# Kernel tuning notes

Hardware: AMD Instinct MI355X
Metric: run time of the kernel (lower is better)

Reference implementation:

```python
import jax, jax.numpy as jnp
import numpy as np

HIDDEN = 512
TEMPERATURE = float(np.sqrt(HIDDEN))  # scaled-dot temperature
BATCH = 64


def _build_weights(attn_weight, N, K):
    """Vectorized version of get_attn_weight: (S,S,H) with S = N*K+1.
    Regions: 0=same_sample, 1=same_class, 2=diff_class, 3=support->query,
    4=query->support, 5=query->query. Replicates the torch overwrite order."""
    S = N * K + 1
    NK = N * K
    i = jnp.arange(S)[:, None]
    j = jnp.arange(S)[None, :]
    idx = jnp.full((S, S), 2, dtype=jnp.int32)                      # w_diff_class
    idx = jnp.where((i // K) == (j // K), 1, idx)                   # w_same_class
    idx = jnp.where((i < NK) & (j == NK), 3, idx)                   # w_stoquery
    idx = jnp.where(i == j, 0, idx)                                 # w_same_sample (diag)
    idx = jnp.where((i == NK) & (j < NK), 4, idx)                   # w_querytos
    idx = jnp.where((i == NK) & (j == NK), 5, idx)                  # w_query
    return attn_weight[idx]  # (S, S, H)


def setup_inputs() -> dict:
    key = jax.random.key(0)
    kq, kk, kv, kw = jax.random.split(key, 4)
    N, K = 10, 10
    S = N * K + 1  # 101
    q = jax.random.normal(kq, (BATCH, S, HIDDEN), dtype=jnp.float32)
    k = jax.random.normal(kk, (BATCH, S, HIDDEN), dtype=jnp.float32)
    v = jax.random.normal(kv, (BATCH, S, HIDDEN), dtype=jnp.float32)
    bound = float(np.sqrt(6 / 2))
    attn_weight = jax.random.uniform(kw, (6, HIDDEN), dtype=jnp.float32,
                                     minval=-bound, maxval=bound)
    return {"q": q, "k": k, "v": v, "attn_weight": attn_weight, "N": N, "K": K}


def reference(q, k, v, attn_weight, N, K):
    # attn[b,i,j] = softmax_j(q.k^T / temperature)
    scores = jnp.einsum("bih,bjh->bij", q, k) / TEMPERATURE
    attn = jax.nn.softmax(scores, axis=2)  # dropout p=0 (eval) -> identity
    weights = _build_weights(attn_weight, N, K)  # (S,S,H)
    # out[b,i,h] = sum_j attn[b,i,j] * weights[i,j,h] * v[b,j,h]
    out = jnp.einsum("bij,ijh,bjh->bih", attn, weights, v)
    return out, attn
```

## Files before the change

### kernel.cpp

```cpp
#include <hip/hip_runtime.h>
#include <math.h>
#include <stdint.h>

#define BATCH 64
#define SEQ   101
#define HID   512
#define NKQ   100
#define KCLS  10
#define INV_TEMP 0.04419417382415922f

typedef short bf16x8 __attribute__((ext_vector_type(8)));
typedef float f32x4  __attribute__((ext_vector_type(4)));
typedef uint32_t u32x4 __attribute__((ext_vector_type(4)));

__device__ inline uint32_t cvt2(float a, float b) {
    uint32_t r;
    asm("v_cvt_pk_bf16_f32 %0, %1, %2" : "=v"(r) : "v"(a), "v"(b));
    return r;
}
__device__ inline void split_bf16(float x, short& hi, short& lo) {
    uint32_t u = __builtin_bit_cast(uint32_t, x);
    hi = (short)(u >> 16);
    float hf = __builtin_bit_cast(float, u & 0xFFFF0000u);
    float l  = x - hf;
    lo = (short)(__builtin_bit_cast(uint32_t, l) >> 16);
}

#define QST 520

#define OFF_QLO 16640
#define POOLSZ  33280

__global__ __launch_bounds__(512, 2)
void fused_attn(const float* __restrict__ q, const float* __restrict__ k,
                const float* __restrict__ v, const float* __restrict__ aw,
                float* __restrict__ out, float* __restrict__ attn) {
    __shared__ __align__(16) char pool[POOLSZ];
    __shared__ __align__(16) float sc[16][132];
    short (*qhi)[QST] = (short(*)[QST])(pool);
    short (*qlo)[QST] = (short(*)[QST])(pool + OFF_QLO);

    const int b   = blockIdx.x & 63;
    const int i0  = (blockIdx.x >> 6) * 16;
    const int tid = threadIdx.x;
    const int wv  = tid >> 6, lane = tid & 63;
    const int m   = lane & 15;
    const int g   = lane >> 4;
    const int kq  = g * 8;
    const int rq  = g * 4;
    const int j0w = wv * 16;

    const float* qb = q + (size_t)b * SEQ * HID;
    const float* kb = k + (size_t)b * SEQ * HID;
    const float* vb = v + (size_t)b * SEQ * HID;

    #pragma unroll
    for (int s = 0; s < 4; ++s) {
        const int f = tid + s * 512;
        const int r = f >> 7, c = (f & 127) << 2;
        const int gi = i0 + r;
        f32x4 x = {};
        if (gi < SEQ) x = *(const f32x4*)(qb + (size_t)gi * HID + c);
        short4 hv, lv;
        split_bf16(x[0], hv.x, lv.x);
        split_bf16(x[1], hv.y, lv.y);
        split_bf16(x[2], hv.z, lv.z);
        split_bf16(x[3], hv.w, lv.w);
        *(short4*)&qhi[r][c] = hv;
        *(short4*)&qlo[r][c] = lv;
    }
    __syncthreads();

    f32x4 acc = {};
    {
        const int jg = j0w + m;
        const int jr = (jg > NKQ) ? NKQ : jg;
        const float* kr = kb + (size_t)jr * HID + kq;
        f32x4 k0 = *(const f32x4*)(kr);
        f32x4 k1 = *(const f32x4*)(kr + 4);
        #pragma unroll
        for (int ks = 0; ks < 16; ++ks) {
            f32x4 n0 = {}, n1 = {};
            if (ks < 15) {
                n0 = *(const f32x4*)(kr + (ks + 1) * 32);
                n1 = *(const f32x4*)(kr + (ks + 1) * 32 + 4);
            }
            u32x4 kp;
            kp[0] = cvt2(k0[0], k0[1]); kp[1] = cvt2(k0[2], k0[3]);
            kp[2] = cvt2(k1[0], k1[1]); kp[3] = cvt2(k1[2], k1[3]);
            const bf16x8 kH = __builtin_bit_cast(bf16x8, kp);
            const bf16x8 qH = *(const bf16x8*)&qhi[m][ks * 32 + kq];
            const bf16x8 qL = *(const bf16x8*)&qlo[m][ks * 32 + kq];
            acc = __builtin_amdgcn_mfma_f32_16x16x32_bf16(qH, kH, acc, 0, 0, 0);
            acc = __builtin_amdgcn_mfma_f32_16x16x32_bf16(qL, kH, acc, 0, 0, 0);
            k0 = n0; k1 = n1;
        }
    }
    #pragma unroll
    for (int r = 0; r < 4; ++r)
        sc[rq + r][j0w + m] = acc[r];
    __syncthreads();

    {
        const int row = tid >> 5, t32 = tid & 31;
        const int gi  = i0 + row;
        float mx = -1e30f;
        for (int j = t32; j < SEQ; j += 32) {
            float s = sc[row][j] * INV_TEMP;
            sc[row][j] = s;
            mx = fmaxf(mx, s);
        }
        #pragma unroll
        for (int off = 1; off < 32; off <<= 1) mx = fmaxf(mx, __shfl_xor(mx, off));
        float sum = 0.f;
        for (int j = t32; j < SEQ; j += 32) {
            float e = __expf(sc[row][j] - mx);
            sc[row][j] = e;
            sum += e;
        }
        #pragma unroll
        for (int off = 1; off < 32; off <<= 1) sum += __shfl_xor(sum, off);
        const float inv = 1.f / sum;
        float* arow = attn + ((size_t)b * SEQ + gi) * SEQ;
        for (int j = t32; j < SEQ; j += 32) {
            float a = sc[row][j] * inv;
            sc[row][j] = a;
            if (gi < SEQ) arow[j] = a;
        }
        for (int j = SEQ + t32; j < 128; j += 32) sc[row][j] = 0.f;
    }
    __syncthreads();

    int ai = i0 + m; if (ai > NKQ) ai = NKQ;
    const int ci = ai / KCLS;
    uint32_t mbits = 0;
    #pragma unroll
    for (int ks = 0; ks < 4; ++ks)
        #pragma unroll
        for (int e = 0; e < 8; ++e)
            if (((ks * 32 + kq + e) / KCLS) == ci) mbits |= (1u << (ks * 8 + e));
    bf16x8 Ah[4], Al[4];
    #pragma unroll
    for (int ks = 0; ks < 4; ++ks) {
        const f32x4 u0 = *(const f32x4*)&sc[m][ks * 32 + kq];
        const f32x4 u1 = *(const f32x4*)&sc[m][ks * 32 + kq + 4];
        const float x[8] = {u0[0], u0[1], u0[2], u0[3], u1[0], u1[1], u1[2], u1[3]};
        #pragma unroll
        for (int e = 0; e < 8; ++e) {
            short h, l; split_bf16(x[e], h, l);
            Ah[ks][e] = h; Al[ks][e] = l;
        }
    }

    const int hl = j0w + m;
    for (int hc = 0; hc < 4; ++hc) {
        const int h = (hc << 7) + hl;
        const float* vh = vb + h;
        f32x4 T = {}, U = {};
        #pragma unroll
        for (int ks = 0; ks < 4; ++ks) {
            float xv[8];
            #pragma unroll
            for (int e = 0; e < 8; ++e) {
                const int j  = ks * 32 + kq + e;
                const int jr = (j > NKQ) ? NKQ : j;
                xv[e] = vh[(size_t)jr * HID];
            }
            u32x4 ph, pl;
            #pragma unroll
            for (int p = 0; p < 4; ++p) {
                const uint32_t h01 = cvt2(xv[2 * p], xv[2 * p + 1]);
                const float r0 = xv[2 * p]     - __builtin_bit_cast(float, h01 << 16);
                const float r1 = xv[2 * p + 1] - __builtin_bit_cast(float, h01 & 0xFFFF0000u);
                ph[p] = h01;
                pl[p] = cvt2(r0, r1);
            }
            const bf16x8 Bh = __builtin_bit_cast(bf16x8, ph);
            const bf16x8 Bl = __builtin_bit_cast(bf16x8, pl);
            bf16x8 Mh;
            #pragma unroll
            for (int e = 0; e < 8; ++e)
                Mh[e] = (mbits & (1u << (ks * 8 + e))) ? Ah[ks][e] : (short)0;
            T = __builtin_amdgcn_mfma_f32_16x16x32_bf16(Ah[ks], Bh, T, 0, 0, 0);
            T = __builtin_amdgcn_mfma_f32_16x16x32_bf16(Ah[ks], Bl, T, 0, 0, 0);
            T = __builtin_amdgcn_mfma_f32_16x16x32_bf16(Al[ks], Bh, T, 0, 0, 0);
            U = __builtin_amdgcn_mfma_f32_16x16x32_bf16(Mh,     Bh, U, 0, 0, 0);
        }
        const float w0 = aw[0 * HID + h], w1 = aw[1 * HID + h], w2 = aw[2 * HID + h];
        const float w3 = aw[3 * HID + h], w4 = aw[4 * HID + h], w5 = aw[5 * HID + h];
        const float vN = vb[(size_t)NKQ * HID + h];
        #pragma unroll
        for (int r = 0; r < 4; ++r) {
            const int i = i0 + rq + r;
            if (i >= SEQ) continue;
            const int il = rq + r;
            const float t = T[r], u = U[r];
            const float aiN = sc[il][NKQ];
            float o;
            if (i < NKQ) {
                const float aii = sc[il][i];
                const float vi  = vb[(size_t)i * HID + h];
                o = w2 * t + (w1 - w2) * u + (w0 - w1) * aii * vi + (w3 - w2) * aiN * vN;
            } else {
                o = w4 * t + (w5 - w4) * aiN * vN;
            }
            out[((size_t)b * SEQ + i) * HID + h] = o;
        }
    }
}

extern "C" void kernel_launch(void* const* d_in, const int* in_sizes, int n_in,
                              void* d_out, int out_size, void* d_ws, size_t ws_size,
                              hipStream_t stream) {
    const float* q  = (const float*)d_in[0];
    const float* k  = (const float*)d_in[1];
    const float* v  = (const float*)d_in[2];
    const float* aw = (const float*)d_in[3];
    float* out  = (float*)d_out;
    float* attn = out + (size_t)BATCH * SEQ * HID;
    (void)d_ws; (void)ws_size;

    fused_attn<<<dim3(448), dim3(512), 0, stream>>>(q, k, v, aw, out, attn);
}
```

Before: 110.6 us.

## Stage V tiles through double-buffered LDS with register prefetch

The attn·V phase stops doing strided scalar global loads of V, one row per element, for each column. Each wave now issues coalesced 16-byte loads of a 32×16 V tile into registers two steps ahead. It writes them into a per-wave double-buffered LDS slot and reads the transposed fragment from there. The four h-chunk × four j-chunk loop is flattened into 16 unrolled steps, so later tiles load while the MFMAs run on the current one. In exchange, LDS use roughly doubles, which may limit occupancy, and the code carries extra register pressure and LDS write/read traffic.

```diff
diff --git a/kernel.cpp b/kernel.cpp
--- a/kernel.cpp
+++ b/kernel.cpp
@@ -27,9 +27,10 @@
 }
 
 #define QST 520
-
-#define OFF_QLO 16640
-#define POOLSZ  33280
+#define SLOTSZ 16384
+#define OFF_QHI 32768
+#define OFF_QLO 49408
+#define POOLSZ  66048
 
 __global__ __launch_bounds__(512, 2)
 void fused_attn(const float* __restrict__ q, const float* __restrict__ k,
@@ -37,7 +38,7 @@
                 float* __restrict__ out, float* __restrict__ attn) {
     __shared__ __align__(16) char pool[POOLSZ];
     __shared__ __align__(16) float sc[16][132];
-    short (*qhi)[QST] = (short(*)[QST])(pool);
+    short (*qhi)[QST] = (short(*)[QST])(pool + OFF_QHI);
     short (*qlo)[QST] = (short(*)[QST])(pool + OFF_QLO);
 
     const int b   = blockIdx.x & 63;
@@ -101,6 +102,26 @@
         sc[rq + r][j0w + m] = acc[r];
     __syncthreads();
 
+    const int fj0 = lane >> 2,        fc0 = lane & 3;
+    const int fj1 = (64 + lane) >> 2, fc1 = (64 + lane) & 3;
+    float* vp0 = (float*)(pool + 0 * SLOTSZ) + wv * 512;
+    float* vp1 = (float*)(pool + 1 * SLOTSZ) + wv * 512;
+    f32x4 pfA[2], pfB[2];
+
+    {
+        const int r0 = (fj0 > NKQ) ? NKQ : fj0;
+        const int r1 = (fj1 > NKQ) ? NKQ : fj1;
+        pfA[0] = *(const f32x4*)(vb + (size_t)r0 * HID + j0w + fc0 * 4);
+        pfA[1] = *(const f32x4*)(vb + (size_t)r1 * HID + j0w + fc1 * 4);
+    }
+    {
+        const int j0 = 32;
+        const int r0 = (j0 + fj0 > NKQ) ? NKQ : j0 + fj0;
+        const int r1 = (j0 + fj1 > NKQ) ? NKQ : j0 + fj1;
+        pfB[0] = *(const f32x4*)(vb + (size_t)r0 * HID + j0w + fc0 * 4);
+        pfB[1] = *(const f32x4*)(vb + (size_t)r1 * HID + j0w + fc1 * 4);
+    }
+
     {
         const int row = tid >> 5, t32 = tid & 31;
         const int gi  = i0 + row;
@@ -152,59 +173,87 @@
         }
     }
 
+    *(f32x4*)(vp0 + lane * 4)        = pfA[0];
+    *(f32x4*)(vp0 + (64 + lane) * 4) = pfA[1];
+
     const int hl = j0w + m;
-    for (int hc = 0; hc < 4; ++hc) {
-        const int h = (hc << 7) + hl;
-        const float* vh = vb + h;
-        f32x4 T = {}, U = {};
-        #pragma unroll
-        for (int ks = 0; ks < 4; ++ks) {
-            float xv[8];
+    f32x4 T = {}, U = {};
+    float w0, w1, w2, w3, w4, w5, vNv, vi_r[4];
+    #pragma unroll
+    for (int s = 0; s < 16; ++s) {
+        const int jc = s & 3, hc = s >> 2;
+        float* vpw = (s & 1) ? vp1 : vp0;
+        float* vpn = (s & 1) ? vp0 : vp1;
+
+        if (s + 1 < 16) {
+            const f32x4* pf = ((s + 1) & 1) ? pfB : pfA;
+            *(f32x4*)(vpn + lane * 4)        = pf[0];
+            *(f32x4*)(vpn + (64 + lane) * 4) = pf[1];
+        }
+        if (s + 2 < 16) {
+            const int nc = s + 2, njc = nc & 3, nhc = nc >> 2;
+            const int j0 = njc * 32, cb = nhc * 128 + j0w;
+            const int r0 = (j0 + fj0 > NKQ) ? NKQ : j0 + fj0;
+            const int r1 = (j0 + fj1 > NKQ) ? NKQ : j0 + fj1;
+            f32x4* pf = ((s + 2) & 1) ? pfB : pfA;
+            pf[0] = *(const f32x4*)(vb + (size_t)r0 * HID + cb + fc0 * 4);
+            pf[1] = *(const f32x4*)(vb + (size_t)r1 * HID + cb + fc1 * 4);
+        }
+        if (jc == 0) {
+            T = (f32x4){}; U = (f32x4){};
+            const int h = (hc << 7) + hl;
+            w0 = aw[0 * HID + h]; w1 = aw[1 * HID + h]; w2 = aw[2 * HID + h];
+            w3 = aw[3 * HID + h]; w4 = aw[4 * HID + h]; w5 = aw[5 * HID + h];
+            vNv = vb[(size_t)NKQ * HID + h];
             #pragma unroll
-            for (int e = 0; e < 8; ++e) {
-                const int j  = ks * 32 + kq + e;
-                const int jr = (j > NKQ) ? NKQ : j;
-                xv[e] = vh[(size_t)jr * HID];
+            for (int r = 0; r < 4; ++r) {
+                const int i = i0 + rq + r;
+                vi_r[r] = (i < NKQ) ? vb[(size_t)i * HID + h] : 0.f;
             }
-            u32x4 ph, pl;
+        }
+        float xv[8];
+        #pragma unroll
+        for (int e = 0; e < 8; ++e)
+            xv[e] = vpw[(kq + e) * 16 + m];
+        u32x4 ph, pl;
+        #pragma unroll
+        for (int p = 0; p < 4; ++p) {
+            const uint32_t h01 = cvt2(xv[2 * p], xv[2 * p + 1]);
+            const float r0 = xv[2 * p]     - __builtin_bit_cast(float, h01 << 16);
+            const float r1 = xv[2 * p + 1] - __builtin_bit_cast(float, h01 & 0xFFFF0000u);
+            ph[p] = h01;
+            pl[p] = cvt2(r0, r1);
+        }
+        const bf16x8 Bh = __builtin_bit_cast(bf16x8, ph);
+        const bf16x8 Bl = __builtin_bit_cast(bf16x8, pl);
+        bf16x8 Mh;
+        #pragma unroll
+        for (int e = 0; e < 8; ++e)
+            Mh[e] = (mbits & (1u << (jc * 8 + e))) ? Ah[jc][e] : (short)0;
+        T = __builtin_amdgcn_mfma_f32_16x16x32_bf16(Ah[jc], Bh, T, 0, 0, 0);
+        T = __builtin_amdgcn_mfma_f32_16x16x32_bf16(Ah[jc], Bl, T, 0, 0, 0);
+        T = __builtin_amdgcn_mfma_f32_16x16x32_bf16(Al[jc], Bh, T, 0, 0, 0);
+        U = __builtin_amdgcn_mfma_f32_16x16x32_bf16(Mh,     Bh, U, 0, 0, 0);
+
+        if (jc == 3) {
+            const int h = (hc << 7) + hl;
             #pragma unroll
-            for (int p = 0; p < 4; ++p) {
-                const uint32_t h01 = cvt2(xv[2 * p], xv[2 * p + 1]);
-                const float r0 = xv[2 * p]     - __builtin_bit_cast(float, h01 << 16);
-                const float r1 = xv[2 * p + 1] - __builtin_bit_cast(float, h01 & 0xFFFF0000u);
-                ph[p] = h01;
-                pl[p] = cvt2(r0, r1);
+            for (int r = 0; r < 4; ++r) {
+                const int i = i0 + rq + r;
+                if (i >= SEQ) continue;
+                const int il = rq + r;
+                const float t = T[r], u = U[r];
+                const float aiN = sc[il][NKQ];
+                float o;
+                if (i < NKQ) {
+                    const float aii = sc[il][i];
+                    o = w2 * t + (w1 - w2) * u + (w0 - w1) * aii * vi_r[r]
+                      + (w3 - w2) * aiN * vNv;
+                } else {
+                    o = w4 * t + (w5 - w4) * aiN * vNv;
+                }
+                out[((size_t)b * SEQ + i) * HID + h] = o;
             }
-            const bf16x8 Bh = __builtin_bit_cast(bf16x8, ph);
-            const bf16x8 Bl = __builtin_bit_cast(bf16x8, pl);
-            bf16x8 Mh;
-            #pragma unroll
-            for (int e = 0; e < 8; ++e)
-                Mh[e] = (mbits & (1u << (ks * 8 + e))) ? Ah[ks][e] : (short)0;
-            T = __builtin_amdgcn_mfma_f32_16x16x32_bf16(Ah[ks], Bh, T, 0, 0, 0);
-            T = __builtin_amdgcn_mfma_f32_16x16x32_bf16(Ah[ks], Bl, T, 0, 0, 0);
-            T = __builtin_amdgcn_mfma_f32_16x16x32_bf16(Al[ks], Bh, T, 0, 0, 0);
-            U = __builtin_amdgcn_mfma_f32_16x16x32_bf16(Mh,     Bh, U, 0, 0, 0);
-        }
-        const float w0 = aw[0 * HID + h], w1 = aw[1 * HID + h], w2 = aw[2 * HID + h];
-        const float w3 = aw[3 * HID + h], w4 = aw[4 * HID + h], w5 = aw[5 * HID + h];
-        const float vN = vb[(size_t)NKQ * HID + h];
-        #pragma unroll
-        for (int r = 0; r < 4; ++r) {
-            const int i = i0 + rq + r;
-            if (i >= SEQ) continue;
-            const int il = rq + r;
-            const float t = T[r], u = U[r];
-            const float aiN = sc[il][NKQ];
-            float o;
-            if (i < NKQ) {
-                const float aii = sc[il][i];
-                const float vi  = vb[(size_t)i * HID + h];
-                o = w2 * t + (w1 - w2) * u + (w0 - w1) * aii * vi + (w3 - w2) * aiN * vN;
-            } else {
-                o = w4 * t + (w5 - w4) * aiN * vN;
-            }
-            out[((size_t)b * SEQ + i) * HID + h] = o;
         }
     }
 }
```

Result: slower. 118.5 us (+7.1%).
